# Kernel optimization log

Hardware: AMD Instinct MI355X
Metric: run time of the kernel (lower is better)

The kernel has to match this reference:

```python
import jax, jax.numpy as jnp
import numpy as np

N_TABLES = 26
VOCAB = 100000
D = 64          # m_spa
B = 16384
L = 4           # fixed pooling factor (uniform offsets)
LN_BOT = [13, 512, 256, 64]
LN_TOP = [415, 512, 256, 1]


def setup_inputs() -> dict:
    key = jax.random.key(0)
    ks = jax.random.split(key, 20)
    inp = {}
    inp["dense_x"] = jax.random.uniform(ks[0], (B, LN_BOT[0]), dtype=jnp.float32)
    # offsets: uniform bags of length L (EmbeddingBag offsets per table)
    inp["lS_o"] = jnp.tile(jnp.arange(B, dtype=jnp.int64) * L, (N_TABLES, 1))
    inp["lS_i"] = jax.random.randint(ks[1], (N_TABLES, B * L), 0, VOCAB, dtype=jnp.int64)
    # embedding tables, uniform(-sqrt(1/n), sqrt(1/n)) as in create_emb
    bound = np.sqrt(1.0 / VOCAB)
    inp["emb"] = jax.random.uniform(ks[2], (N_TABLES, VOCAB, D), dtype=jnp.float32,
                                     minval=-bound, maxval=bound)
    # MLP params, normal init as in create_mlp
    def mk_mlp(ln, k0):
        Ws, bs = [], []
        for i in range(len(ln) - 1):
            n, m = ln[i], ln[i + 1]
            kw, kb = jax.random.split(jax.random.fold_in(k0, i))
            Ws.append(jax.random.normal(kw, (m, n), dtype=jnp.float32) * np.sqrt(2.0 / (m + n)))
            bs.append(jax.random.normal(kb, (m,), dtype=jnp.float32) * np.sqrt(1.0 / m))
        return Ws, bs
    bW, bb = mk_mlp(LN_BOT, ks[3])
    tW, tb = mk_mlp(LN_TOP, ks[4])
    for i in range(3):
        inp[f"bot_W{i}"], inp[f"bot_b{i}"] = bW[i], bb[i]
        inp[f"top_W{i}"], inp[f"top_b{i}"] = tW[i], tb[i]
    return inp


def _lower_tri_pairs(n):
    # li/lj from interact_features with offset=0: all (i, j) with j < i
    li = np.array([i for i in range(n) for j in range(i)])
    lj = np.array([j for i in range(n) for j in range(i)])
    return li, lj


def dlrm_forward(dense_x, lS_i, emb, bot_W, bot_b, top_W, top_b):
    # bottom MLP: Linear + ReLU (sigmoid_bot = -1)
    x = dense_x
    for W, b in zip(bot_W, bot_b):
        x = jax.nn.relu(x @ W.T + b)
    # EmbeddingBag sum pooling: gather rows then sum over bag (fixed L)
    idx = lS_i.reshape(N_TABLES, B, L)                 # [T,B,L]
    # vmap over tables: emb[t][idx[t]] -> [B,L,D] -> sum -> [B,D]
    ly = jax.vmap(lambda tbl, ix: tbl[ix].sum(axis=1))(emb, idx)  # [T,B,D]
    # dot interaction: T = [x] + ly along feature axis -> [B, 1+T, D]
    Tmat = jnp.concatenate([x[:, None, :], jnp.transpose(ly, (1, 0, 2))], axis=1)
    Z = jnp.einsum("bid,bjd->bij", Tmat, Tmat)         # [B, 27, 27]
    li, lj = _lower_tri_pairs(Tmat.shape[1])
    Zflat = Z[:, li, lj]                                # [B, 351]
    R = jnp.concatenate([x, Zflat], axis=1)             # [B, 415]
    # top MLP: ReLU, ReLU, Sigmoid (sigmoid_top = 2)
    z = R
    for i, (W, b) in enumerate(zip(top_W, top_b)):
        z = z @ W.T + b
        z = jax.nn.sigmoid(z) if i == len(top_W) - 1 else jax.nn.relu(z)
    return z  # loss_threshold == 0 -> no clamp


def reference(dense_x, lS_o, lS_i, emb,
              bot_W0, bot_b0, bot_W1, bot_b1, bot_W2, bot_b2,
              top_W0, top_b0, top_W1, top_b1, top_W2, top_b2):
    # lS_o encodes uniform bags of length L; structure is honored via reshape.
    del lS_o
    return dlrm_forward(dense_x, lS_i, emb,
                        [bot_W0, bot_W1, bot_W2], [bot_b0, bot_b1, bot_b2],
                        [top_W0, top_W1, top_W2], [top_b0, top_b1, top_b2])
```

## Files before the change

kernel.cpp:

```cpp
#include <hip/hip_runtime.h>
#include <hip/hip_bf16.h>
#include <cmath>

#define BATCH   16384
#define NT      26
#define VOCAB_N 100000
#define EMB_D   64
#define LOOK    4

typedef __attribute__((ext_vector_type(8))) short  short8;
typedef __attribute__((ext_vector_type(4))) float  float4v;

#define GLOBAL_AS __attribute__((address_space(1)))
#define LDS_AS    __attribute__((address_space(3)))

__global__ __launch_bounds__(256) void conv_bf16(
    const float* __restrict__ in, __hip_bfloat16* __restrict__ out, int n)
{
    int i = blockIdx.x * 256 + threadIdx.x;
    if (i < n) out[i] = __float2bfloat16(in[i]);
}

__global__ __launch_bounds__(256) void conv_bf16_pad(
    const float* __restrict__ in, __hip_bfloat16* __restrict__ out,
    int N, int Kin, int Kout)
{
    int i = blockIdx.x * 256 + threadIdx.x;
    if (i < N * Kout) {
        int r = i / Kout, k = i % Kout;
        out[i] = __float2bfloat16(k < Kin ? in[(size_t)r * Kin + k] : 0.f);
    }
}

__global__ __launch_bounds__(256) void gemm_f32_k13(
    const float* __restrict__ X, const float* __restrict__ W,
    const float* __restrict__ bias, __hip_bfloat16* __restrict__ Y,
    int M, int N, int K)
{
    constexpr int BM = 128, BN = 128, BK = 16, TM = 8, TN = 8, PAD = 4;
    __shared__ __align__(16) float Xs[BK][BM + PAD];
    __shared__ __align__(16) float Ws[BK][BN + PAD];

    const int tid = threadIdx.x;
    const int tx  = tid % (BN / TN);
    const int ty  = tid / (BN / TN);
    const int m0  = blockIdx.y * BM;
    const int n0  = blockIdx.x * BN;

    float acc[TM][TN];
    #pragma unroll
    for (int i = 0; i < TM; i++)
        #pragma unroll
        for (int j = 0; j < TN; j++) acc[i][j] = 0.f;

    for (int k0 = 0; k0 < K; k0 += BK) {
        for (int idx = tid; idx < BM * BK; idx += 256) {
            int r = idx / BK, k = idx % BK, gk = k0 + k;
            Xs[k][r] = (gk < K) ? X[(size_t)(m0 + r) * K + gk] : 0.f;
        }
        for (int idx = tid; idx < BN * BK; idx += 256) {
            int r = idx / BK, k = idx % BK, gk = k0 + k;
            Ws[k][r] = (gk < K) ? W[(size_t)(n0 + r) * K + gk] : 0.f;
        }
        __syncthreads();
        #pragma unroll
        for (int kk = 0; kk < BK; kk++) {
            float a[TM], bb[TN];
            #pragma unroll
            for (int i = 0; i < TM; i++) a[i] = Xs[kk][ty * TM + i];
            #pragma unroll
            for (int j = 0; j < TN; j++) bb[j] = Ws[kk][tx * TN + j];
            #pragma unroll
            for (int i = 0; i < TM; i++)
                #pragma unroll
                for (int j = 0; j < TN; j++)
                    acc[i][j] += a[i] * bb[j];
        }
        __syncthreads();
    }
    #pragma unroll
    for (int i = 0; i < TM; i++) {
        int m = m0 + ty * TM + i;
        #pragma unroll
        for (int j = 0; j < TN; j++) {
            int n = n0 + tx * TN + j;
            float v = fmaxf(acc[i][j] + bias[n], 0.f);
            Y[(size_t)m * N + n] = __float2bfloat16(v);
        }
    }
}

template<int BN, int WM, int WN, int RELU, int OUT_BF16>
__global__ __launch_bounds__(256) void mfma_gemm(
    const short* __restrict__ A, const short* __restrict__ W,
    const float* __restrict__ bias, void* __restrict__ Y,
    int M, int N, int K)
{
    constexpr int BM = 128, BK = 32;
    constexpr int FM = BM / WM / 16;
    constexpr int FN = BN / WN / 16;
    constexpr int ACH = (BM * BK * 2) / 1024;
    constexpr int BCH = (BN * BK * 2) / 1024;

    __shared__ short As[BM * BK];
    __shared__ short Bs[BN * BK];

    const int tid  = threadIdx.x;
    const int wave = tid >> 6;
    const int lane = tid & 63;
    const int wm   = wave / WN;
    const int wn   = wave % WN;
    const int m0   = blockIdx.y * BM;
    const int n0   = blockIdx.x * BN;

    const int r16 = lane >> 2;
    const int c16 = (lane & 3) * 8;

    float4v acc[FM][FN];
    #pragma unroll
    for (int i = 0; i < FM; i++)
        #pragma unroll
        for (int j = 0; j < FN; j++) acc[i][j] = (float4v)(0.f);

    for (int k0 = 0; k0 < K; k0 += BK) {
        #pragma unroll
        for (int c = 0; c < ACH / 4; c++) {
            int chunk = wave * (ACH / 4) + c;
            int row   = chunk * 16 + r16;
            const short* src = A + (size_t)(m0 + row) * K + k0 + c16;
            __builtin_amdgcn_global_load_lds(
                (const GLOBAL_AS void*)src,
                (LDS_AS void*)(As + chunk * 512), 16, 0, 0);
        }
        #pragma unroll
        for (int c = 0; c < BCH / 4; c++) {
            int chunk = wave * (BCH / 4) + c;
            int row   = chunk * 16 + r16;
            const short* src = W + (size_t)(n0 + row) * K + k0 + c16;
            __builtin_amdgcn_global_load_lds(
                (const GLOBAL_AS void*)src,
                (LDS_AS void*)(Bs + chunk * 512), 16, 0, 0);
        }
        __syncthreads();

        short8 a_frag[FM], b_frag[FN];
        const int kq = (lane >> 4) * 8;
        #pragma unroll
        for (int fi = 0; fi < FM; fi++) {
            int m_local = wm * (BM / WM) + fi * 16 + (lane & 15);
            a_frag[fi] = *(const short8*)(As + m_local * BK + kq);
        }
        #pragma unroll
        for (int fj = 0; fj < FN; fj++) {
            int n_local = wn * (BN / WN) + fj * 16 + (lane & 15);
            b_frag[fj] = *(const short8*)(Bs + n_local * BK + kq);
        }
        #pragma unroll
        for (int fi = 0; fi < FM; fi++)
            #pragma unroll
            for (int fj = 0; fj < FN; fj++)
                acc[fi][fj] = __builtin_amdgcn_mfma_f32_16x16x32_bf16(
                    a_frag[fi], b_frag[fj], acc[fi][fj], 0, 0, 0);

        __syncthreads();
    }

    #pragma unroll
    for (int fi = 0; fi < FM; fi++) {
        #pragma unroll
        for (int fj = 0; fj < FN; fj++) {
            int col   = n0 + wn * (BN / WN) + fj * 16 + (lane & 15);
            int rbase = m0 + wm * (BM / WM) + fi * 16 + (lane >> 4) * 4;
            float bv  = bias[col];
            #pragma unroll
            for (int r = 0; r < 4; r++) {
                float v = acc[fi][fj][r] + bv;
                if (RELU) v = fmaxf(v, 0.f);
                if (OUT_BF16)
                    ((__hip_bfloat16*)Y)[(size_t)(rbase + r) * N + col] =
                        __float2bfloat16(v);
                else
                    ((float*)Y)[(size_t)(rbase + r) * N + col] = v;
            }
        }
    }
}

#define TS 68

__global__ __launch_bounds__(256) void interact_kernel(
    const float* __restrict__ x2,
    const int*   __restrict__ lS_i,
    const float* __restrict__ emb,
    __hip_bfloat16* __restrict__ R)
{
    __shared__ __align__(16) float T[(NT + 1) * TS];
    __shared__ int sidx[NT * LOOK];

    const int b   = blockIdx.x;
    const int tid = threadIdx.x;

    if (tid < NT * LOOK) {
        int tb = tid >> 2, l = tid & 3;
        sidx[tid] = lS_i[(size_t)tb * (BATCH * LOOK) + (size_t)b * LOOK + l];
    }
    if (tid < EMB_D) T[tid] = x2[(size_t)b * EMB_D + tid];
    __syncthreads();

    const int d = tid & 63;
    for (int tb = tid >> 6; tb < NT; tb += 4) {
        float s = 0.f;
        #pragma unroll
        for (int l = 0; l < LOOK; l++) {
            int row = sidx[tb * LOOK + l];
            s += emb[((size_t)tb * VOCAB_N + row) * EMB_D + d];
        }
        T[(tb + 1) * TS + d] = s;
    }
    __syncthreads();

    __hip_bfloat16* Rb = R + (size_t)b * 416;
    if (tid < EMB_D) Rb[tid] = __float2bfloat16(T[tid]);
    if (tid == 64)  Rb[415] = __float2bfloat16(0.f);

    for (int p = tid; p < 351; p += 256) {
        int i = (int)((1.0f + sqrtf(1.0f + 8.0f * (float)p)) * 0.5f);
        while (i * (i - 1) / 2 > p) --i;
        while ((i + 1) * i / 2 <= p) ++i;
        int j = p - i * (i - 1) / 2;
        const float* Ti = &T[i * TS];
        const float* Tj = &T[j * TS];
        float s = 0.f;
        #pragma unroll
        for (int k = 0; k < EMB_D; k++) s += Ti[k] * Tj[k];
        Rb[64 + p] = __float2bfloat16(s);
    }
}

__global__ __launch_bounds__(256) void top_final(
    const float* __restrict__ z1, const float* __restrict__ W2,
    const float* __restrict__ b2, float* __restrict__ out)
{
    const int wave = threadIdx.x >> 6;
    const int lane = threadIdx.x & 63;
    const int b = blockIdx.x * 4 + wave;

    float s = 0.f;
    #pragma unroll
    for (int q = 0; q < 4; q++) {
        int k = q * 64 + lane;
        s += z1[(size_t)b * 256 + k] * W2[k];
    }
    #pragma unroll
    for (int off = 32; off; off >>= 1) s += __shfl_down(s, off, 64);
    if (lane == 0) out[b] = 1.f / (1.f + expf(-(s + b2[0])));
}

extern "C" void kernel_launch(void* const* d_in, const int* in_sizes, int n_in,
                              void* d_out, int out_size, void* d_ws, size_t ws_size,
                              hipStream_t stream)
{
    const float* dense = (const float*)d_in[0];
    const int*   lS_i  = (const int*)d_in[2];
    const float* emb   = (const float*)d_in[3];
    const float* bW0 = (const float*)d_in[4];  const float* bb0 = (const float*)d_in[5];
    const float* tW0 = (const float*)d_in[6];  const float* tb0 = (const float*)d_in[7];
    const float* bW1 = (const float*)d_in[8];  const float* bb1 = (const float*)d_in[9];
    const float* tW1 = (const float*)d_in[10]; const float* tb1 = (const float*)d_in[11];
    const float* bW2 = (const float*)d_in[12]; const float* bb2 = (const float*)d_in[13];
    const float* tW2 = (const float*)d_in[14]; const float* tb2 = (const float*)d_in[15];
    float* out = (float*)d_out;

    char* p = (char*)d_ws;
    __hip_bfloat16* x0_bf = (__hip_bfloat16*)p;  p += (size_t)BATCH * 512 * 2;
    __hip_bfloat16* x1_bf = (__hip_bfloat16*)p;  p += (size_t)BATCH * 256 * 2;
    float*          x2_f  = (float*)p;           p += (size_t)BATCH * 64  * 4;
    __hip_bfloat16* R_bf  = (__hip_bfloat16*)p;  p += (size_t)BATCH * 416 * 2;
    __hip_bfloat16* z0_bf = (__hip_bfloat16*)p;  p += (size_t)BATCH * 512 * 2;
    float*          z1_f  = (float*)p;           p += (size_t)BATCH * 256 * 4;
    __hip_bfloat16* wb1   = (__hip_bfloat16*)p;  p += (size_t)256 * 512 * 2;
    __hip_bfloat16* wb2   = (__hip_bfloat16*)p;  p += (size_t)64  * 256 * 2;
    __hip_bfloat16* wt0   = (__hip_bfloat16*)p;  p += (size_t)512 * 416 * 2;
    __hip_bfloat16* wt1   = (__hip_bfloat16*)p;  p += (size_t)256 * 512 * 2;

    dim3 blk(256);

    conv_bf16<<<dim3((256 * 512 + 255) / 256), blk, 0, stream>>>(bW1, wb1, 256 * 512);
    conv_bf16<<<dim3((64 * 256 + 255) / 256),  blk, 0, stream>>>(bW2, wb2, 64 * 256);
    conv_bf16_pad<<<dim3((512 * 416 + 255) / 256), blk, 0, stream>>>(tW0, wt0, 512, 415, 416);
    conv_bf16<<<dim3((256 * 512 + 255) / 256), blk, 0, stream>>>(tW1, wt1, 256 * 512);

    gemm_f32_k13<<<dim3(512 / 128, BATCH / 128), blk, 0, stream>>>(
        dense, bW0, bb0, x0_bf, BATCH, 512, 13);
    mfma_gemm<128, 2, 2, 1, 1><<<dim3(256 / 128, BATCH / 128), blk, 0, stream>>>(
        (const short*)x0_bf, (const short*)wb1, bb1, x1_bf, BATCH, 256, 512);
    mfma_gemm<64, 4, 1, 1, 0><<<dim3(1, BATCH / 128), blk, 0, stream>>>(
        (const short*)x1_bf, (const short*)wb2, bb2, x2_f, BATCH, 64, 256);

    interact_kernel<<<dim3(BATCH), blk, 0, stream>>>(x2_f, lS_i, emb, R_bf);

    mfma_gemm<128, 2, 2, 1, 1><<<dim3(512 / 128, BATCH / 128), blk, 0, stream>>>(
        (const short*)R_bf, (const short*)wt0, tb0, z0_bf, BATCH, 512, 416);
    mfma_gemm<128, 2, 2, 1, 0><<<dim3(256 / 128, BATCH / 128), blk, 0, stream>>>(
        (const short*)z0_bf, (const short*)wt1, tb1, z1_f, BATCH, 256, 512);
    top_final<<<dim3(BATCH / 4), blk, 0, stream>>>(z1_f, tW2, tb2, out);
}
```

Baseline: 904.9 us.

## Compute pairwise interaction with split-bf16 MFMA and vectorize embedding gathers

Replaces the scalar per-pair 64-length dot products in the interaction kernel with MFMA 16x16x32 bf16 tiles, splitting each fp32 value into hi and lo bf16 parts and summing three products to approximate fp32 accuracy. Embedding bag gathers now use float4 loads with 16 threads per table row, and the four weight conversion launches are merged into one kernel. The aim is to cut ALU and LDS work in the interaction stage and reduce launch overhead. The hi/lo split drops the lo*lo term, which introduces a small precision difference.

```diff
diff --git a/kernel.cpp b/kernel.cpp
--- a/kernel.cpp
+++ b/kernel.cpp
@@ -14,22 +14,33 @@
 #define GLOBAL_AS __attribute__((address_space(1)))
 #define LDS_AS    __attribute__((address_space(3)))
 
-__global__ __launch_bounds__(256) void conv_bf16(
-    const float* __restrict__ in, __hip_bfloat16* __restrict__ out, int n)
+static __device__ __forceinline__ short f32_to_bf16_bits(float f) {
+    unsigned u = __builtin_bit_cast(unsigned, f);
+    unsigned r = (u + 0x7fffu + ((u >> 16) & 1u)) >> 16;
+    return (short)r;
+}
+static __device__ __forceinline__ float bf16_bits_to_f32(short s) {
+    return __builtin_bit_cast(float, ((unsigned)(unsigned short)s) << 16);
+}
+
+__global__ __launch_bounds__(256) void conv_all(
+    const float* __restrict__ bW1, const float* __restrict__ bW2,
+    const float* __restrict__ tW0, const float* __restrict__ tW1,
+    __hip_bfloat16* __restrict__ wb1, __hip_bfloat16* __restrict__ wb2,
+    __hip_bfloat16* __restrict__ wt0, __hip_bfloat16* __restrict__ wt1)
 {
     int i = blockIdx.x * 256 + threadIdx.x;
-    if (i < n) out[i] = __float2bfloat16(in[i]);
-}
-
-__global__ __launch_bounds__(256) void conv_bf16_pad(
-    const float* __restrict__ in, __hip_bfloat16* __restrict__ out,
-    int N, int Kin, int Kout)
-{
-    int i = blockIdx.x * 256 + threadIdx.x;
-    if (i < N * Kout) {
-        int r = i / Kout, k = i % Kout;
-        out[i] = __float2bfloat16(k < Kin ? in[(size_t)r * Kin + k] : 0.f);
-    }
+    if (i < 131072) { wb1[i] = __float2bfloat16(bW1[i]); return; }
+    i -= 131072;
+    if (i < 16384)  { wb2[i] = __float2bfloat16(bW2[i]); return; }
+    i -= 16384;
+    if (i < 212992) {
+        int r = i / 416, k = i % 416;
+        wt0[i] = __float2bfloat16(k < 415 ? tW0[(size_t)r * 415 + k] : 0.f);
+        return;
+    }
+    i -= 212992;
+    if (i < 131072) wt1[i] = __float2bfloat16(tW1[i]);
 }
 
 __global__ __launch_bounds__(256) void gemm_f32_k13(
@@ -194,7 +205,7 @@
     const float* __restrict__ emb,
     __hip_bfloat16* __restrict__ R)
 {
-    __shared__ __align__(16) float T[(NT + 1) * TS];
+    __shared__ __align__(16) float T[32 * TS];
     __shared__ int sidx[NT * LOOK];
 
     const int b   = blockIdx.x;
@@ -204,36 +215,84 @@
         int tb = tid >> 2, l = tid & 3;
         sidx[tid] = lS_i[(size_t)tb * (BATCH * LOOK) + (size_t)b * LOOK + l];
     }
-    if (tid < EMB_D) T[tid] = x2[(size_t)b * EMB_D + tid];
+    if (tid < 16) {
+        *(float4*)(&T[tid * 4]) = *(const float4*)(x2 + (size_t)b * EMB_D + tid * 4);
+    }
+    for (int i = 27 * TS + tid; i < 32 * TS; i += 256) T[i] = 0.f;
     __syncthreads();
 
-    const int d = tid & 63;
-    for (int tb = tid >> 6; tb < NT; tb += 4) {
-        float s = 0.f;
-        #pragma unroll
-        for (int l = 0; l < LOOK; l++) {
-            int row = sidx[tb * LOOK + l];
-            s += emb[((size_t)tb * VOCAB_N + row) * EMB_D + d];
-        }
-        T[(tb + 1) * TS + d] = s;
+    const int c4 = (tid & 15) * 4;
+    #pragma unroll
+    for (int it = 0; it < 2; ++it) {
+        int tb = (tid >> 4) + it * 16;
+        if (tb < NT) {
+            float4 s = {0.f, 0.f, 0.f, 0.f};
+            #pragma unroll
+            for (int l = 0; l < LOOK; l++) {
+                int row = sidx[tb * LOOK + l];
+                float4 v = *(const float4*)(emb +
+                    ((size_t)tb * VOCAB_N + row) * EMB_D + c4);
+                s.x += v.x; s.y += v.y; s.z += v.z; s.w += v.w;
+            }
+            *(float4*)(&T[(tb + 1) * TS + c4]) = s;
+        }
     }
     __syncthreads();
 
+    const int wave = tid >> 6;
+    const int lane = tid & 63;
     __hip_bfloat16* Rb = R + (size_t)b * 416;
-    if (tid < EMB_D) Rb[tid] = __float2bfloat16(T[tid]);
-    if (tid == 64)  Rb[415] = __float2bfloat16(0.f);
-
-    for (int p = tid; p < 351; p += 256) {
-        int i = (int)((1.0f + sqrtf(1.0f + 8.0f * (float)p)) * 0.5f);
-        while (i * (i - 1) / 2 > p) --i;
-        while ((i + 1) * i / 2 <= p) ++i;
-        int j = p - i * (i - 1) / 2;
-        const float* Ti = &T[i * TS];
-        const float* Tj = &T[j * TS];
-        float s = 0.f;
-        #pragma unroll
-        for (int k = 0; k < EMB_D; k++) s += Ti[k] * Tj[k];
-        Rb[64 + p] = __float2bfloat16(s);
+
+    if (wave < 3) {
+        const int ti = (wave == 0) ? 0 : 1;
+        const int tj = (wave == 2) ? 1 : 0;
+
+        short8 fhi[2][2], flo[2][2];
+        const int r  = lane & 15;
+        const int kq = (lane >> 4) * 8;
+        #pragma unroll
+        for (int rt = 0; rt < 2; rt++) {
+            #pragma unroll
+            for (int kk = 0; kk < 2; kk++) {
+                const float* src = &T[(rt * 16 + r) * TS + kk * 32 + kq];
+                float4 v0 = *(const float4*)(src);
+                float4 v1 = *(const float4*)(src + 4);
+                float vv[8] = {v0.x, v0.y, v0.z, v0.w, v1.x, v1.y, v1.z, v1.w};
+                short8 h, l;
+                #pragma unroll
+                for (int j = 0; j < 8; j++) {
+                    short hb = f32_to_bf16_bits(vv[j]);
+                    float hf = bf16_bits_to_f32(hb);
+                    short lb = f32_to_bf16_bits(vv[j] - hf);
+                    h[j] = hb; l[j] = lb;
+                }
+                fhi[rt][kk] = h; flo[rt][kk] = l;
+            }
+        }
+
+        float4v acc = (float4v)(0.f);
+        #pragma unroll
+        for (int kk = 0; kk < 2; kk++) {
+            acc = __builtin_amdgcn_mfma_f32_16x16x32_bf16(
+                      fhi[ti][kk], fhi[tj][kk], acc, 0, 0, 0);
+            acc = __builtin_amdgcn_mfma_f32_16x16x32_bf16(
+                      fhi[ti][kk], flo[tj][kk], acc, 0, 0, 0);
+            acc = __builtin_amdgcn_mfma_f32_16x16x32_bf16(
+                      flo[ti][kk], fhi[tj][kk], acc, 0, 0, 0);
+        }
+
+        const int gj = tj * 16 + (lane & 15);
+        #pragma unroll
+        for (int rr = 0; rr < 4; rr++) {
+            int gi = ti * 16 + (lane >> 4) * 4 + rr;
+            if (gi < NT + 1 && gi > gj) {
+                int p = gi * (gi - 1) / 2 + gj;
+                Rb[64 + p] = __float2bfloat16(acc[rr]);
+            }
+        }
+    } else {
+        Rb[lane] = __float2bfloat16(T[lane]);
+        if (lane == 0) Rb[415] = __float2bfloat16(0.f);
     }
 }
 
@@ -285,10 +344,7 @@
 
     dim3 blk(256);
 
-    conv_bf16<<<dim3((256 * 512 + 255) / 256), blk, 0, stream>>>(bW1, wb1, 256 * 512);
-    conv_bf16<<<dim3((64 * 256 + 255) / 256),  blk, 0, stream>>>(bW2, wb2, 64 * 256);
-    conv_bf16_pad<<<dim3((512 * 416 + 255) / 256), blk, 0, stream>>>(tW0, wt0, 512, 415, 416);
-    conv_bf16<<<dim3((256 * 512 + 255) / 256), blk, 0, stream>>>(tW1, wt1, 256 * 512);
+    conv_all<<<dim3(1920), blk, 0, stream>>>(bW1, bW2, tW0, tW1, wb1, wb2, wt0, wt1);
 
     gemm_f32_k13<<<dim3(512 / 128, BATCH / 128), blk, 0, stream>>>(
         dense, bW0, bb0, x0_bf, BATCH, 512, 13);
```

After: 895.9 us. Within noise of the previous version (-1.0%).
